# Performance work log

Hardware: AMD Instinct MI355X
Metric: run time of the kernel (lower is better)

## Reference

```python
import jax, jax.numpy as jnp
import numpy as np

B, T, I, H = 2048, 256, 64, 64  # batch, seq_len, input_size, hidden_size


def setup_inputs() -> dict:
    key = jax.random.key(0)
    ks = jax.random.split(key, 11)
    w = lambda k, shape: (jax.random.normal(k, shape, jnp.float32) * 0.05)
    return {
        "x": jax.random.normal(ks[0], (B, T, I), jnp.float32),
        # layer 0 (input -> hidden), PyTorch gate order [i, f, g, o] stacked along dim 0
        "W_ih0": w(ks[1], (4 * H, I)),
        "W_hh0": w(ks[2], (4 * H, H)),
        "b_ih0": w(ks[3], (4 * H,)),
        "b_hh0": w(ks[4], (4 * H,)),
        # layer 1 (hidden -> hidden)
        "W_ih1": w(ks[5], (4 * H, H)),
        "W_hh1": w(ks[6], (4 * H, H)),
        "b_ih1": w(ks[7], (4 * H,)),
        "b_hh1": w(ks[8], (4 * H,)),
        # final projection hidden -> 1
        "fc_w": w(ks[9], (1, H)),
        "fc_b": w(ks[10], (1,)),
    }


def _lstm_layer(x, W_ih, W_hh, b_ih, b_hh):
    """Single LSTM layer, batch_first input (B, T, D) -> (B, T, H).
    PyTorch gate order: i, f, g, o."""
    Bsz, Tlen, _ = x.shape
    Hd = W_hh.shape[1]
    # Precompute input projections for all timesteps in one big GEMM.
    x_proj = jnp.einsum("btd,gd->btg", x, W_ih) + b_ih + b_hh  # (B, T, 4H)
    x_proj = jnp.swapaxes(x_proj, 0, 1)  # (T, B, 4H) for scan over time

    def step(carry, xt):
        h, c = carry
        gates = xt + h @ W_hh.T  # (B, 4H)
        i, f, g, o = jnp.split(gates, 4, axis=-1)
        i = jax.nn.sigmoid(i)
        f = jax.nn.sigmoid(f)
        g = jnp.tanh(g)
        o = jax.nn.sigmoid(o)
        c = f * c + i * g
        h = o * jnp.tanh(c)
        return (h, c), h

    h0 = jnp.zeros((Bsz, Hd), x.dtype)
    (_, _), hs = jax.lax.scan(step, (h0, h0), x_proj)
    return jnp.swapaxes(hs, 0, 1)  # (B, T, H)


def reference(x, W_ih0, W_hh0, b_ih0, b_hh0, W_ih1, W_hh1, b_ih1, b_hh1, fc_w, fc_b):
    # Dropout between layers is inactive in eval mode -> omitted.
    h1 = _lstm_layer(x, W_ih0, W_hh0, b_ih0, b_hh0)
    h2 = _lstm_layer(h1, W_ih1, W_hh1, b_ih1, b_hh1)
    last_hidden = h2[:, -1, :]  # (B, H)
    out = last_hidden @ fc_w.T + fc_b  # (B, 1)
    return out[:, 0]  # squeeze(-1) -> (B,)
```

## Files before the change

kernel.cpp:

```cpp
#include <hip/hip_runtime.h>

typedef short short8 __attribute__((ext_vector_type(8)));
typedef float f32x4  __attribute__((ext_vector_type(4)));
typedef unsigned short u16;

#define T_LEN 256
#define NB    8
#define GRID  (2048 / NB)
#define LDK   72

static __device__ __forceinline__ u16 bf16_rne(float f) {
    unsigned u = __builtin_bit_cast(unsigned, f);
    return (u16)((u + 0x7fffu + ((u >> 16) & 1u)) >> 16);
}
static __device__ __forceinline__ float bf16_f(u16 h) {
    unsigned u = ((unsigned)h) << 16;
    return __builtin_bit_cast(float, u);
}
static __device__ __forceinline__ void split_tr(float f, u16& hi, u16& lo) {
    unsigned u = __builtin_bit_cast(unsigned, f);
    hi = (u16)(u >> 16);
    float rest = f - __builtin_bit_cast(float, u & 0xffff0000u);
    lo = (u16)(__builtin_bit_cast(unsigned, rest) >> 16);
}
static __device__ __forceinline__ float fast_sigmoid(float x) {
    float e = __builtin_amdgcn_exp2f(x * -1.4426950408889634f);
    return __builtin_amdgcn_rcpf(1.0f + e);
}
static __device__ __forceinline__ float fast_tanh(float x) {
    float e = __builtin_amdgcn_exp2f(x * -2.8853900817779268f);
    return 2.0f * __builtin_amdgcn_rcpf(1.0f + e) - 1.0f;
}

__global__ __launch_bounds__(1024)
void lstm2_mfma(const float* __restrict__ x,
                const float* __restrict__ W_ih0, const float* __restrict__ W_hh0,
                const float* __restrict__ b_ih0, const float* __restrict__ b_hh0,
                const float* __restrict__ W_ih1, const float* __restrict__ W_hh1,
                const float* __restrict__ b_ih1, const float* __restrict__ b_hh1,
                const float* __restrict__ fc_w,  const float* __restrict__ fc_b,
                float* __restrict__ out)
{
    const int tid = threadIdx.x;
    const int l   = tid & 63;
    const int w   = tid >> 6;
    const int grp = w >> 3;
    const int wl  = w & 7;
    const int ln  = l & 15;
    const int kg  = l >> 4;

    __shared__ __align__(16) u16 XB[2][16][LDK];
    __shared__ __align__(16) u16 H1[2][16][LDK];
    __shared__ __align__(16) u16 H2[2][16][LDK];
    __shared__ __align__(16) float hfin[NB][68];

    short8 Ah[2][4], Al[2][4];
    f32x4  biasv[2];
    {
        const float* Wi = grp ? W_ih1 : W_ih0;
        const float* Wh = grp ? W_hh1 : W_hh0;
        const float* bi = grp ? b_ih1 : b_ih0;
        const float* bh = grp ? b_hh1 : b_hh0;
        #pragma unroll
        for (int mt = 0; mt < 2; ++mt) {
            #pragma unroll
            for (int kt = 0; kt < 4; ++kt) {
                const int uu   = ln >> 2;
                const int gate = ln & 3;
                const int row  = gate * 64 + (wl * 8 + mt * 4 + uu);
                const int kb   = kt * 32 + kg * 8;
                const float* src = (kb < 64) ? (Wi + (size_t)row * 64 + kb)
                                             : (Wh + (size_t)row * 64 + (kb - 64));
                short8 h8, l8;
                #pragma unroll
                for (int j = 0; j < 8; ++j) {
                    float v = src[j];
                    u16 hh = bf16_rne(v);
                    u16 ll = bf16_rne(v - bf16_f(hh));
                    h8[j] = (short)hh; l8[j] = (short)ll;
                }
                Ah[mt][kt] = h8; Al[mt][kt] = l8;
            }
            f32x4 bv;
            #pragma unroll
            for (int r = 0; r < 4; ++r) {
                const int row = r * 64 + (wl * 8 + mt * 4 + kg);
                bv[r] = bi[row] + bh[row];
            }
            biasv[mt] = bv;
        }
    }

    {
        u16* p0 = &XB[0][0][0];
        u16* p1 = &H1[0][0][0];
        u16* p2 = &H2[0][0][0];
        const int tot = 2 * 16 * LDK;
        for (int i = tid; i < tot; i += 1024) { p0[i] = 0; p1[i] = 0; p2[i] = 0; }
    }
    __syncthreads();

    const int    sb    = blockIdx.x * NB;
    const bool   stg   = (grp == 1);
    const int    xs    = wl;
    const int    xj    = l;
    const size_t xbase = ((size_t)(sb + xs)) * T_LEN * 64 + xj;

    if (stg) {
        u16 hh, ll; split_tr(x[xbase], hh, ll);
        XB[0][xs][xj]     = hh;
        XB[0][8 + xs][xj] = ll;
    }
    __syncthreads();

    const int  mtl  = (ln >> 3) & 1;
    const int  smp  = ln & 7;
    const int  un   = wl * 8 + mtl * 4 + kg;
    const bool lo8  = (ln < 8);
    const f32x4 zv  = {0.f, 0.f, 0.f, 0.f};
    const f32x4 init0 = lo8 ? biasv[0] : zv;
    const f32x4 init1 = lo8 ? biasv[1] : zv;
    float cstate = 0.f;
    float xcur = stg ? x[xbase + 64] : 0.f;

#define MFMA(A, B, C) __builtin_amdgcn_mfma_f32_16x16x32_bf16(A, B, C, 0, 0, 0)

#define STEPB(T, P, G0, G1, STG_ON, XLOAD, FIN)                              \
    do {                                                                     \
        float xnext_ = 0.f;                                                  \
        if ((XLOAD) && stg) xnext_ = x[xbase + (size_t)((T) + 2) * 64];      \
        const bool act_ = grp ? (bool)(G1) : (bool)(G0);                     \
        if (act_) {                                                          \
            short8 b0, b1, b2, b3;                                           \
            if (grp) {                                                       \
                b0 = *(const short8*)&H1[P][ln][kg * 8];                     \
                b1 = *(const short8*)&H1[P][ln][32 + kg * 8];                \
                b2 = *(const short8*)&H2[P][ln][kg * 8];                     \
                b3 = *(const short8*)&H2[P][ln][32 + kg * 8];                \
            } else {                                                         \
                b0 = *(const short8*)&XB[P][ln][kg * 8];                     \
                b1 = *(const short8*)&XB[P][ln][32 + kg * 8];                \
                b2 = *(const short8*)&H1[P][ln][kg * 8];                     \
                b3 = *(const short8*)&H1[P][ln][32 + kg * 8];                \
            }                                                                \
            f32x4 a0 = init0, a1 = init1;                                    \
            a0 = MFMA(Ah[0][0], b0, a0);  a1 = MFMA(Ah[1][0], b0, a1);       \
            a0 = MFMA(Al[0][0], b0, a0);  a1 = MFMA(Al[1][0], b0, a1);       \
            a0 = MFMA(Ah[0][1], b1, a0);  a1 = MFMA(Ah[1][1], b1, a1);       \
            a0 = MFMA(Al[0][1], b1, a0);  a1 = MFMA(Al[1][1], b1, a1);       \
            a0 = MFMA(Ah[0][2], b2, a0);  a1 = MFMA(Ah[1][2], b2, a1);       \
            a0 = MFMA(Al[0][2], b2, a0);  a1 = MFMA(Al[1][2], b2, a1);       \
            a0 = MFMA(Ah[0][3], b3, a0);  a1 = MFMA(Ah[1][3], b3, a1);       \
            a0 = MFMA(Al[0][3], b3, a0);  a1 = MFMA(Al[1][3], b3, a1);       \
            f32x4 pk;                                                        \
            _Pragma("unroll")                                                \
            for (int r = 0; r < 4; ++r) {                                    \
                float send_ = lo8 ? a1[r] : a0[r];            \
                int   si_   = __builtin_bit_cast(int, send_);                \
                int   ri_   = __builtin_amdgcn_mov_dpp(si_, 0x128, 0xf, 0xf, \
                                                       true);     \
                float recv_ = __builtin_bit_cast(float, ri_);                \
                float self_ = lo8 ? a0[r] : a1[r];                           \
                pk[r] = self_ + recv_;                                       \
            }                                                                \
            const float ig = fast_sigmoid(pk[0]);                            \
            const float fg = fast_sigmoid(pk[1]);                            \
            const float gg = fast_tanh(pk[2]);                               \
            const float og = fast_sigmoid(pk[3]);                            \
            const float cc = fg * cstate + ig * gg;                          \
            cstate = cc;                                                     \
            const float hv = og * fast_tanh(cc);                             \
            u16 hh_, ll_; split_tr(hv, hh_, ll_);                            \
            if (grp == 0) {                                                  \
                H1[1 - (P)][smp][un]     = hh_;                              \
                H1[1 - (P)][8 + smp][un] = ll_;                              \
            } else {                                                         \
                H2[1 - (P)][smp][un]     = hh_;                              \
                H2[1 - (P)][8 + smp][un] = ll_;                              \
                if (FIN) hfin[smp][un] = hv;                                 \
            }                                                                \
        }                                                                    \
        if ((STG_ON) && stg) {                                               \
            u16 hh_, ll_; split_tr(xcur, hh_, ll_);                          \
            XB[1 - (P)][xs][xj]     = hh_;                                   \
            XB[1 - (P)][8 + xs][xj] = ll_;                                   \
        }                                                                    \
        xcur = xnext_;                                                       \
        __syncthreads();                                                     \
    } while (0)

    STEPB(0, 0, 1, 0, 1, 1, 0);
    #pragma unroll 1
    for (int t = 1; t <= 251; t += 2) {
        STEPB(t,     1, 1, 1, 1, 1, 0);
        STEPB(t + 1, 0, 1, 1, 1, 1, 0);
    }
    STEPB(253, 1, 1, 1, 1, 1, 0);
    STEPB(254, 0, 1, 1, 1, 0, 0);
    STEPB(255, 1, 1, 1, 0, 0, 0);
    STEPB(256, 0, 0, 1, 0, 0, 1);
#undef STEPB
#undef MFMA

    if (w < 8) {
        float v = hfin[w][l] * fc_w[l];
        #pragma unroll
        for (int off = 32; off; off >>= 1) v += __shfl_xor(v, off, 64);
        if (l == 0) out[sb + w] = v + fc_b[0];
    }
}

extern "C" void kernel_launch(void* const* d_in, const int* in_sizes, int n_in,
                              void* d_out, int out_size, void* d_ws, size_t ws_size,
                              hipStream_t stream) {
    const float* x     = (const float*)d_in[0];
    const float* W_ih0 = (const float*)d_in[1];
    const float* W_hh0 = (const float*)d_in[2];
    const float* b_ih0 = (const float*)d_in[3];
    const float* b_hh0 = (const float*)d_in[4];
    const float* W_ih1 = (const float*)d_in[5];
    const float* W_hh1 = (const float*)d_in[6];
    const float* b_ih1 = (const float*)d_in[7];
    const float* b_hh1 = (const float*)d_in[8];
    const float* fc_w  = (const float*)d_in[9];
    const float* fc_b  = (const float*)d_in[10];
    float* out = (float*)d_out;

    lstm2_mfma<<<GRID, 1024, 0, stream>>>(x, W_ih0, W_hh0, b_ih0, b_hh0,
                                          W_ih1, W_hh1, b_ih1, b_hh1,
                                          fc_w, fc_b, out);
}
```

Baseline: 238.5 us.

## Split each LSTM step into two phases so both layers' MFMA and activation alternate

Each timestep now has two barrier-separated phases. Layer 0 runs its MFMAs while layer 1 runs the activations from its previous MFMA, then the roles swap. Layer 1's activation is deferred by half a step, so H2 no longer needs double buffering and becomes a single buffer. The aim is to overlap matrix and transcendental work across the two wave groups on the critical path, at the cost of doubling the number of __syncthreads per step.

```diff
diff --git a/kernel.cpp b/kernel.cpp
--- a/kernel.cpp
+++ b/kernel.cpp
@@ -51,7 +51,7 @@
 
     __shared__ __align__(16) u16 XB[2][16][LDK];
     __shared__ __align__(16) u16 H1[2][16][LDK];
-    __shared__ __align__(16) u16 H2[2][16][LDK];
+    __shared__ __align__(16) u16 H2[16][LDK];
     __shared__ __align__(16) float hfin[NB][68];
 
     short8 Ah[2][4], Al[2][4];
@@ -94,9 +94,11 @@
     {
         u16* p0 = &XB[0][0][0];
         u16* p1 = &H1[0][0][0];
-        u16* p2 = &H2[0][0][0];
-        const int tot = 2 * 16 * LDK;
-        for (int i = tid; i < tot; i += 1024) { p0[i] = 0; p1[i] = 0; p2[i] = 0; }
+        const int tot2 = 2 * 16 * LDK;
+        for (int i = tid; i < tot2; i += 1024) { p0[i] = 0; p1[i] = 0; }
+        u16* p2 = &H2[0][0];
+        const int tot1 = 16 * LDK;
+        for (int i = tid; i < tot1; i += 1024) p2[i] = 0;
     }
     __syncthreads();
 
@@ -121,28 +123,12 @@
     const f32x4 init0 = lo8 ? biasv[0] : zv;
     const f32x4 init1 = lo8 ? biasv[1] : zv;
     float cstate = 0.f;
+    f32x4 pk = zv;
     float xcur = stg ? x[xbase + 64] : 0.f;
 
 #define MFMA(A, B, C) __builtin_amdgcn_mfma_f32_16x16x32_bf16(A, B, C, 0, 0, 0)
 
-#define STEPB(T, P, G0, G1, STG_ON, XLOAD, FIN)                              \
-    do {                                                                     \
-        float xnext_ = 0.f;                                                  \
-        if ((XLOAD) && stg) xnext_ = x[xbase + (size_t)((T) + 2) * 64];      \
-        const bool act_ = grp ? (bool)(G1) : (bool)(G0);                     \
-        if (act_) {                                                          \
-            short8 b0, b1, b2, b3;                                           \
-            if (grp) {                                                       \
-                b0 = *(const short8*)&H1[P][ln][kg * 8];                     \
-                b1 = *(const short8*)&H1[P][ln][32 + kg * 8];                \
-                b2 = *(const short8*)&H2[P][ln][kg * 8];                     \
-                b3 = *(const short8*)&H2[P][ln][32 + kg * 8];                \
-            } else {                                                         \
-                b0 = *(const short8*)&XB[P][ln][kg * 8];                     \
-                b1 = *(const short8*)&XB[P][ln][32 + kg * 8];                \
-                b2 = *(const short8*)&H1[P][ln][kg * 8];                     \
-                b3 = *(const short8*)&H1[P][ln][32 + kg * 8];                \
-            }                                                                \
+#define MFMA16(b0, b1, b2, b3)                                               \
             f32x4 a0 = init0, a1 = init1;                                    \
             a0 = MFMA(Ah[0][0], b0, a0);  a1 = MFMA(Ah[1][0], b0, a1);       \
             a0 = MFMA(Al[0][0], b0, a0);  a1 = MFMA(Al[1][0], b0, a1);       \
@@ -152,7 +138,6 @@
             a0 = MFMA(Al[0][2], b2, a0);  a1 = MFMA(Al[1][2], b2, a1);       \
             a0 = MFMA(Ah[0][3], b3, a0);  a1 = MFMA(Ah[1][3], b3, a1);       \
             a0 = MFMA(Al[0][3], b3, a0);  a1 = MFMA(Al[1][3], b3, a1);       \
-            f32x4 pk;                                                        \
             _Pragma("unroll")                                                \
             for (int r = 0; r < 4; ++r) {                                    \
                 float send_ = lo8 ? a1[r] : a0[r];            \
@@ -162,44 +147,81 @@
                 float recv_ = __builtin_bit_cast(float, ri_);                \
                 float self_ = lo8 ? a0[r] : a1[r];                           \
                 pk[r] = self_ + recv_;                                       \
-            }                                                                \
-            const float ig = fast_sigmoid(pk[0]);                            \
-            const float fg = fast_sigmoid(pk[1]);                            \
-            const float gg = fast_tanh(pk[2]);                               \
-            const float og = fast_sigmoid(pk[3]);                            \
-            const float cc = fg * cstate + ig * gg;                          \
-            cstate = cc;                                                     \
-            const float hv = og * fast_tanh(cc);                             \
-            u16 hh_, ll_; split_tr(hv, hh_, ll_);                            \
-            if (grp == 0) {                                                  \
+            }
+
+#define ACTBODY                                                              \
+            const float ig_ = fast_sigmoid(pk[0]);                           \
+            const float fg_ = fast_sigmoid(pk[1]);                           \
+            const float gg_ = fast_tanh(pk[2]);                              \
+            const float og_ = fast_sigmoid(pk[3]);                           \
+            const float cc_ = fg_ * cstate + ig_ * gg_;                      \
+            cstate = cc_;                                                    \
+            const float hv_ = og_ * fast_tanh(cc_);                          \
+            u16 hh_, ll_; split_tr(hv_, hh_, ll_)
+
+#define STEP2(T, P, G0, G1M, G1A, STG_ON, XLOAD, FIN)                        \
+    do {                                                                     \
+        float xnext_ = 0.f;                                                  \
+                                    \
+        if (grp == 0) {                                                      \
+            if (G0) {                                                        \
+                short8 b0 = *(const short8*)&XB[P][ln][kg * 8];              \
+                short8 b1 = *(const short8*)&XB[P][ln][32 + kg * 8];         \
+                short8 b2 = *(const short8*)&H1[P][ln][kg * 8];              \
+                short8 b3 = *(const short8*)&H1[P][ln][32 + kg * 8];         \
+                MFMA16(b0, b1, b2, b3);                                      \
+            }                                                                \
+        } else {                                                             \
+            if (XLOAD) xnext_ = x[xbase + (size_t)((T) + 2) * 64];           \
+            if (G1A) {                                  \
+                ACTBODY;                                                     \
+                H2[smp][un]     = hh_;                                       \
+                H2[8 + smp][un] = ll_;                                       \
+                if (FIN) hfin[smp][un] = hv_;                                \
+            }                                                                \
+            if (STG_ON) {                                  \
+                u16 hh_, ll_; split_tr(xcur, hh_, ll_);                      \
+                XB[1 - (P)][xs][xj]     = hh_;                               \
+                XB[1 - (P)][8 + xs][xj] = ll_;                               \
+            }                                                                \
+        }                                                                    \
+        __syncthreads();                                                     \
+                                    \
+        if (grp == 0) {                                                      \
+            if (G0) {                              \
+                ACTBODY;                                                     \
                 H1[1 - (P)][smp][un]     = hh_;                              \
                 H1[1 - (P)][8 + smp][un] = ll_;                              \
-            } else {                                                         \
-                H2[1 - (P)][smp][un]     = hh_;                              \
-                H2[1 - (P)][8 + smp][un] = ll_;                              \
-                if (FIN) hfin[smp][un] = hv;                                 \
-            }                                                                \
+            }                                                                \
+        } else {                                                             \
+            if (G1M) {                             \
+                short8 b0 = *(const short8*)&H1[P][ln][kg * 8];              \
+                short8 b1 = *(const short8*)&H1[P][ln][32 + kg * 8];         \
+                short8 b2 = *(const short8*)&H2[ln][kg * 8];                 \
+                short8 b3 = *(const short8*)&H2[ln][32 + kg * 8];            \
+                MFMA16(b0, b1, b2, b3);                                      \
+            }                                                                \
+            xcur = xnext_;                                                   \
         }                                                                    \
-        if ((STG_ON) && stg) {                                               \
-            u16 hh_, ll_; split_tr(xcur, hh_, ll_);                          \
-            XB[1 - (P)][xs][xj]     = hh_;                                   \
-            XB[1 - (P)][8 + xs][xj] = ll_;                                   \
-        }                                                                    \
-        xcur = xnext_;                                                       \
         __syncthreads();                                                     \
     } while (0)
 
-    STEPB(0, 0, 1, 0, 1, 1, 0);
+    STEP2(0, 0, 1, 0, 0, 1, 1, 0);
+    STEP2(1, 1, 1, 1, 0, 1, 1, 0);
+    STEP2(2, 0, 1, 1, 1, 1, 1, 0);
     #pragma unroll 1
-    for (int t = 1; t <= 251; t += 2) {
-        STEPB(t,     1, 1, 1, 1, 1, 0);
-        STEPB(t + 1, 0, 1, 1, 1, 1, 0);
-    }
-    STEPB(253, 1, 1, 1, 1, 1, 0);
-    STEPB(254, 0, 1, 1, 1, 0, 0);
-    STEPB(255, 1, 1, 1, 0, 0, 0);
-    STEPB(256, 0, 0, 1, 0, 0, 1);
-#undef STEPB
+    for (int t = 3; t <= 251; t += 2) {
+        STEP2(t,     1, 1, 1, 1, 1, 1, 0);
+        STEP2(t + 1, 0, 1, 1, 1, 1, 1, 0);
+    }
+    STEP2(253, 1, 1, 1, 1, 1, 1, 0);
+    STEP2(254, 0, 1, 1, 1, 1, 0, 0);
+    STEP2(255, 1, 1, 1, 1, 0, 0, 0);
+    STEP2(256, 0, 0, 1, 1, 0, 0, 0);
+    STEP2(257, 1, 0, 0, 1, 0, 0, 1);
+#undef STEP2
+#undef ACTBODY
+#undef MFMA16
 #undef MFMA
 
     if (w < 8) {
```

Result: no change. 238.3 us (-0.1%).
